# Kernel optimization log

Hardware: AMD Instinct MI355X
Metric: run time of the kernel (lower is better)

The kernel has to match this reference:

```python
import jax, jax.numpy as jnp
import numpy as np

PATCH = 3
ALPHA = 0.1


def _unfold3x3(x):
    # x: [B, C, H, W] -> [B, C*9, H, W], torch F.unfold with k=3, pad=1, stride=1
    B, C, H, W = x.shape
    p = PATCH // 2
    xp = jnp.pad(x, ((0, 0), (0, 0), (p, p), (p, p)))
    shifts = [xp[:, :, i:i + H, j:j + W] for i in range(PATCH) for j in range(PATCH)]
    # torch unfold orders (C, kh, kw); ordering is irrelevant for the dot-product
    # correlation, but we match it anyway: stack kernel positions after channel.
    out = jnp.stack(shifts, axis=2)  # [B, C, 9, H, W]
    return out.reshape(B, C * PATCH * PATCH, H, W)


def setup_inputs() -> dict:
    key = jax.random.key(0)
    k1, k2 = jax.random.split(key)
    x_lab = jax.random.normal(k1, (4, 3, 64, 64), dtype=jnp.float32)
    feature = jax.random.normal(k2, (4, 64, 64, 64), dtype=jnp.float32)
    return {"x_lab": x_lab, "feature": feature}


def reference(x_lab, feature):
    # scale_factor=1 and feature already at (H, W): both interpolates are identity.
    B, _, H, W = x_lab.shape
    N = H * W
    x_ab = x_lab.reshape(B, 3, N).transpose(0, 2, 1)          # [B, N, 3]
    lf = _unfold3x3(feature).reshape(B, -1, N)                 # [B, C*9, N]
    corr = jnp.einsum('bcn,bcm->bnm', lf, lf)                  # [B, N, N]
    attn = jax.nn.softmax(corr / ALPHA, axis=-1)
    weighted = jnp.einsum('bnm,bmc->bnc', attn, x_ab)          # [B, N, 3]
    return weighted.transpose(0, 2, 1).reshape(B, 3, H, W)
```

## Files before the change

kernel.cpp:

```cpp
#include <hip/hip_runtime.h>


#define NPIX 4096
#define ROWCH 528
#define ROWB  (ROWCH * 16)
#define SCALE 10.0f

typedef __attribute__((ext_vector_type(8))) short bf16x8;
typedef __attribute__((ext_vector_type(4))) float f32x4;

#define MF(a, b, c) __builtin_amdgcn_mfma_f32_16x16x32_bf16(a, b, c, 0, 0, 0)

__device__ __forceinline__ uint4 pack8(const float* v) {
    unsigned h[8];
#pragma unroll
    for (int j = 0; j < 8; ++j) {
        unsigned u = __float_as_uint(v[j]);
        u = u + 0x7fffu + ((u >> 16) & 1u);
        h[j] = u >> 16;
    }
    return (uint4){h[0] | (h[1] << 16), h[2] | (h[3] << 16),
                   h[4] | (h[5] << 16), h[6] | (h[7] << 16)};
}

__device__ __forceinline__ void load_row(const float* fr, int kc, int x, float* L) {
#pragma unroll
    for (int j = 0; j < 8; ++j) L[j] = fr[(size_t)(kc * 8 + j) * NPIX + x];
}

#define MFMA_GRP(T, DBASE) do {                                               \
    _Pragma("unroll")                                                         \
    for (int dx = 0; dx < 3; ++dx)                                            \
        _Pragma("unroll")                                                     \
        for (int ks = 0; ks < 2; ++ks) {                                      \
            acc[T][0] = MF(AF[((DBASE) + dx) * 2 + ks], Bf[ks][0][dx], acc[T][0]); \
            acc[T][1] = MF(AF[((DBASE) + dx) * 2 + ks], Bf[ks][1][dx], acc[T][1]); \
        }                                                                     \
} while (0)

#define RETIRE(S, myv) do {                                                   \
    _Pragma("unroll")                                                         \
    for (int kt = 0; kt < 2; ++kt) {                                          \
        const int kx = kh * 32 + kt * 16 + nl;                                \
        const float xv0 = xls[(myv) * 64 + kx];                               \
        const float xv1 = xls[NPIX + (myv) * 64 + kx];                        \
        const float xv2 = xls[2 * NPIX + (myv) * 64 + kx];                    \
        _Pragma("unroll")                                                     \
        for (int rg = 0; rg < 4; ++rg) {                                      \
            const float e = __expf(fmaf(acc[S][kt][rg], SCALE, negM[rg]));    \
            l_[rg] += e;                                                      \
            A0[rg] = fmaf(e, xv0, A0[rg]);                                    \
            A1[rg] = fmaf(e, xv1, A1[rg]);                                    \
            A2[rg] = fmaf(e, xv2, A2[rg]);                                    \
        }                                                                     \
        acc[S][kt] = (f32x4){0.f, 0.f, 0.f, 0.f};                             \
    }                                                                         \
} while (0)

#define STEP(RM, SN, SR, rr) do {                                             \
    const int r_ = (rr);                                                      \
    if (r_ <= 61) *(uint4*)(ring + (SR) * ROWB + wu16) = pack8(L);            \
    if (r_ <= 60) load_row(featb + (r_ + 3) * 64, kc, x, L);                  \
    if (r_ < 64) {                                                            \
        const char* base = ring + (RM) * ROWB + bu;                           \
        bf16x8 Bf[2][2][3];                                                   \
        _Pragma("unroll")                                                     \
        for (int ks = 0; ks < 2; ++ks)                                        \
            _Pragma("unroll")                                                 \
            for (int kt = 0; kt < 2; ++kt) {                                  \
                const char* p = base + (ks * 264 + kt * 16) * 16;             \
                Bf[ks][kt][0] = *(const bf16x8*)(p);                          \
                Bf[ks][kt][1] = *(const bf16x8*)(p + 16);                     \
                Bf[ks][kt][2] = *(const bf16x8*)(p + 32);                     \
            }                                                                 \
        if (r_ >= 1)     MFMA_GRP(SR, 6);           \
        MFMA_GRP(RM, 3);                                    \
        if (r_ + 1 < 64) MFMA_GRP(SN, 0);                   \
    }                                                                         \
    if (r_ >= 1 && r_ <= 64) RETIRE(SR, r_ - 1);                              \
    if (r_ < 64) __syncthreads();                                             \
} while (0)

__global__ __launch_bounds__(512)
__attribute__((amdgpu_waves_per_eu(2, 2)))
void nlwa_fused(const float* __restrict__ x_lab,
                const float* __restrict__ feature,
                float* __restrict__ out)
{
    __shared__ __align__(16) char ring[3 * ROWB];
    __shared__ float xls[3 * NPIX];
    __shared__ float part[3][8][64];
    __shared__ float ssq[3][64];
    __shared__ float4 scrF[64][2];

    const int tid = threadIdx.x;
    const int b = blockIdx.x >> 6, ny = blockIdx.x & 63;
    const int w = tid >> 6, lane = tid & 63;
    const int quad = lane >> 4, nl = lane & 15;
    const int qw = w & 3, kh = w >> 2;
    const int kc = w, x = lane;
    const int wu16 = (kc * 66 + x + 1) * 16;
    const int bu = (quad * 66 + kh * 32 + nl) * 16;

    const float* featb = feature + (size_t)b * 64 * NPIX;
    const float* xb = x_lab + (size_t)b * 3 * NPIX;

    {
        const float4* s4 = (const float4*)xb;
        float4* d4 = (float4*)xls;
        for (int i = tid; i < 3 * NPIX / 4; i += 512) d4[i] = s4[i];
    }
    if (tid < 48) {
        const int sl = tid / 16, pu = tid % 16;
        const int u = (pu >> 1) * 66 + (pu & 1) * 65;
        *(uint4*)(ring + sl * ROWB + u * 16) = (uint4){0u, 0u, 0u, 0u};
    }

    float L[8];
#pragma unroll
    for (int dyi = 0; dyi < 3; ++dyi) {
        const int qr = ny + dyi - 1;
        float ss = 0.f;
        if (qr >= 0 && qr < 64) {
            load_row(featb + qr * 64, kc, x, L);
#pragma unroll
            for (int j = 0; j < 8; ++j) ss = fmaf(L[j], L[j], ss);
            *(uint4*)(ring + dyi * ROWB + wu16) = pack8(L);
        } else {
            *(uint4*)(ring + dyi * ROWB + wu16) = (uint4){0u, 0u, 0u, 0u};
        }
        part[dyi][kc][x] = ss;
    }
    __syncthreads();

    if (tid < 192) {
        const int dyi = tid >> 6, xx = tid & 63;
        float s = 0.f;
#pragma unroll
        for (int k = 0; k < 8; ++k) s += part[dyi][k][xx];
        ssq[dyi][xx] = s;
    }

    bf16x8 AF[18];
#pragma unroll
    for (int dyi = 0; dyi < 3; ++dyi)
#pragma unroll
        for (int dx = 0; dx < 3; ++dx)
#pragma unroll
            for (int ks = 0; ks < 2; ++ks)
                AF[(dyi * 3 + dx) * 2 + ks] = *(const bf16x8*)(ring + dyi * ROWB +
                    ((quad + ks * 4) * 66 + qw * 16 + nl + dx) * 16);
    __syncthreads();

    float negM[4];
#pragma unroll
    for (int rg = 0; rg < 4; ++rg) {
        const int q = qw * 16 + quad * 4 + rg;
        float a = 0.f;
#pragma unroll
        for (int dyi = 0; dyi < 3; ++dyi)
#pragma unroll
            for (int dx = -1; dx <= 1; ++dx) {
                const int cx = q + dx;
                a += (cx >= 0 && cx < 64) ? ssq[dyi][cx] : 0.f;
            }
        negM[rg] = -SCALE * a;
    }

#pragma unroll
    for (int rr = 0; rr < 2; ++rr) {
        load_row(featb + rr * 64, kc, x, L);
        *(uint4*)(ring + rr * ROWB + wu16) = pack8(L);
    }
    load_row(featb + 2 * 64, kc, x, L);

    float l_[4], A0[4], A1[4], A2[4];
#pragma unroll
    for (int rg = 0; rg < 4; ++rg) { l_[rg] = 0.f; A0[rg] = 0.f; A1[rg] = 0.f; A2[rg] = 0.f; }
    f32x4 acc[3][2];
#pragma unroll
    for (int i = 0; i < 3; ++i) {
        acc[i][0] = (f32x4){0.f, 0.f, 0.f, 0.f};
        acc[i][1] = (f32x4){0.f, 0.f, 0.f, 0.f};
    }
    __syncthreads();

    for (int rb = 0; rb < 66; rb += 3) {
        STEP(0, 1, 2, rb);
        STEP(1, 2, 0, rb + 1);
        STEP(2, 0, 1, rb + 2);
    }

#pragma unroll
    for (int rg = 0; rg < 4; ++rg) {
#pragma unroll
        for (int off = 8; off >= 1; off >>= 1) {
            l_[rg] += __shfl_down(l_[rg], off, 16);
            A0[rg] += __shfl_down(A0[rg], off, 16);
            A1[rg] += __shfl_down(A1[rg], off, 16);
            A2[rg] += __shfl_down(A2[rg], off, 16);
        }
    }
    if (nl == 0) {
#pragma unroll
        for (int rg = 0; rg < 4; ++rg) {
            const int q = qw * 16 + quad * 4 + rg;
            scrF[q][kh] = make_float4(l_[rg], A0[rg], A1[rg], A2[rg]);
        }
    }
    __syncthreads();
    if (tid < 64) {
        const float4 t0 = scrF[tid][0], t1 = scrF[tid][1];
        const float inv = 1.0f / (t0.x + t1.x);
        float* o = out + (size_t)b * 3 * NPIX + ny * 64 + tid;
        o[0]        = (t0.y + t1.y) * inv;
        o[NPIX]     = (t0.z + t1.z) * inv;
        o[2 * NPIX] = (t0.w + t1.w) * inv;
    }
}

extern "C" void kernel_launch(void* const* d_in, const int* in_sizes, int n_in,
                              void* d_out, int out_size, void* d_ws, size_t ws_size,
                              hipStream_t stream) {
    (void)in_sizes; (void)n_in; (void)out_size; (void)d_ws; (void)ws_size;
    const float* x_lab   = (const float*)d_in[0];
    const float* feature = (const float*)d_in[1];
    float* out = (float*)d_out;
    nlwa_fused<<<dim3(256), dim3(512), 0, stream>>>(x_lab, feature, out);
}
```

Before: 134.3 us.

## Split key rows across two blocks per query row and combine partials

Each query row is now handled by two blocks, each covering half of the key rows (32 of 64). Each block writes unnormalized softmax sums and weighted accumulators to the workspace, and a second small kernel adds the two halves and normalizes. This doubles the grid from 256 to 512 blocks to fill more of the CUs, and the waves-per-EU hint is raised to match. The cost is a second launch, a workspace round trip, and recomputing the halo and norms in both halves. Because the max is a fixed bound taken from the norms, the two partial sums can be added directly.

```diff
diff --git a/kernel.cpp b/kernel.cpp
--- a/kernel.cpp
+++ b/kernel.cpp
@@ -5,6 +5,7 @@
 #define ROWCH 528
 #define ROWB  (ROWCH * 16)
 #define SCALE 10.0f
+#define XCH   2048
 
 typedef __attribute__((ext_vector_type(8))) short bf16x8;
 typedef __attribute__((ext_vector_type(4))) float f32x4;
@@ -43,8 +44,8 @@
     for (int kt = 0; kt < 2; ++kt) {                                          \
         const int kx = kh * 32 + kt * 16 + nl;                                \
         const float xv0 = xls[(myv) * 64 + kx];                               \
-        const float xv1 = xls[NPIX + (myv) * 64 + kx];                        \
-        const float xv2 = xls[2 * NPIX + (myv) * 64 + kx];                    \
+        const float xv1 = xls[XCH + (myv) * 64 + kx];                         \
+        const float xv2 = xls[2 * XCH + (myv) * 64 + kx];                     \
         _Pragma("unroll")                                                     \
         for (int rg = 0; rg < 4; ++rg) {                                      \
             const float e = __expf(fmaf(acc[S][kt][rg], SCALE, negM[rg]));    \
@@ -57,11 +58,15 @@
     }                                                                         \
 } while (0)
 
-#define STEP(RM, SN, SR, rr) do {                                             \
-    const int r_ = (rr);                                                      \
-    if (r_ <= 61) *(uint4*)(ring + (SR) * ROWB + wu16) = pack8(L);            \
-    if (r_ <= 60) load_row(featb + (r_ + 3) * 64, kc, x, L);                  \
-    if (r_ < 64) {                                                            \
+#define STEP(RM, SN, SR, tt) do {                                             \
+    const int t_ = (tt);                                                      \
+    if (t_ <= 31) *(uint4*)(ring + (SR) * ROWB + wu16) = pack8(L);            \
+    if (t_ <= 30) {                                                           \
+        const int g3 = K0 + 2 + t_;                                           \
+        if (g3 < 64) { load_row(featb + g3 * 64, kc, x, L); }                 \
+        else { _Pragma("unroll") for (int j = 0; j < 8; ++j) L[j] = 0.f; }    \
+    }                                                                         \
+    if (t_ <= 33) {                                                           \
         const char* base = ring + (RM) * ROWB + bu;                           \
         bf16x8 Bf[2][2][3];                                                   \
         _Pragma("unroll")                                                     \
@@ -73,28 +78,31 @@
                 Bf[ks][kt][1] = *(const bf16x8*)(p + 16);                     \
                 Bf[ks][kt][2] = *(const bf16x8*)(p + 32);                     \
             }                                                                 \
-        if (r_ >= 1)     MFMA_GRP(SR, 6);           \
-        MFMA_GRP(RM, 3);                                    \
-        if (r_ + 1 < 64) MFMA_GRP(SN, 0);                   \
+        if (t_ >= 2)              MFMA_GRP(SR, 6);    \
+        if (t_ >= 1 && t_ <= 32)  MFMA_GRP(RM, 3);          \
+        if (t_ <= 31)             MFMA_GRP(SN, 0);          \
     }                                                                         \
-    if (r_ >= 1 && r_ <= 64) RETIRE(SR, r_ - 1);                              \
-    if (r_ < 64) __syncthreads();                                             \
+    if (t_ >= 2 && t_ <= 33) RETIRE(SR, t_ - 2);                              \
+    if (t_ <= 33) __syncthreads();                                            \
 } while (0)
 
 __global__ __launch_bounds__(512)
-__attribute__((amdgpu_waves_per_eu(2, 2)))
+__attribute__((amdgpu_waves_per_eu(4, 4)))
 void nlwa_fused(const float* __restrict__ x_lab,
                 const float* __restrict__ feature,
-                float* __restrict__ out)
+                float4* __restrict__ ws)
 {
     __shared__ __align__(16) char ring[3 * ROWB];
-    __shared__ float xls[3 * NPIX];
+    __shared__ float xls[3 * XCH];
     __shared__ float part[3][8][64];
     __shared__ float ssq[3][64];
     __shared__ float4 scrF[64][2];
 
     const int tid = threadIdx.x;
-    const int b = blockIdx.x >> 6, ny = blockIdx.x & 63;
+    const int b = blockIdx.x >> 7;
+    const int r7 = blockIdx.x & 127;
+    const int ny = r7 >> 1, half = r7 & 1;
+    const int K0 = half * 32;
     const int w = tid >> 6, lane = tid & 63;
     const int quad = lane >> 4, nl = lane & 15;
     const int qw = w & 3, kh = w >> 2;
@@ -106,9 +114,12 @@
     const float* xb = x_lab + (size_t)b * 3 * NPIX;
 
     {
-        const float4* s4 = (const float4*)xb;
+        const int base = K0 * 64;
         float4* d4 = (float4*)xls;
-        for (int i = tid; i < 3 * NPIX / 4; i += 512) d4[i] = s4[i];
+        for (int i = tid; i < 3 * XCH / 4; i += 512) {
+            const int ch = i >> 9, off = i & 511;
+            d4[i] = *(const float4*)(xb + (size_t)ch * NPIX + base + off * 4);
+        }
     }
     if (tid < 48) {
         const int sl = tid / 16, pu = tid % 16;
@@ -169,10 +180,15 @@
 
 #pragma unroll
     for (int rr = 0; rr < 2; ++rr) {
-        load_row(featb + rr * 64, kc, x, L);
-        *(uint4*)(ring + rr * ROWB + wu16) = pack8(L);
-    }
-    load_row(featb + 2 * 64, kc, x, L);
+        const int g = K0 - 1 + rr;
+        if (g >= 0) {
+            load_row(featb + g * 64, kc, x, L);
+            *(uint4*)(ring + rr * ROWB + wu16) = pack8(L);
+        } else {
+            *(uint4*)(ring + rr * ROWB + wu16) = (uint4){0u, 0u, 0u, 0u};
+        }
+    }
+    load_row(featb + (K0 + 1) * 64, kc, x, L);
 
     float l_[4], A0[4], A1[4], A2[4];
 #pragma unroll
@@ -185,7 +201,7 @@
     }
     __syncthreads();
 
-    for (int rb = 0; rb < 66; rb += 3) {
+    for (int rb = 0; rb < 36; rb += 3) {
         STEP(0, 1, 2, rb);
         STEP(1, 2, 0, rb + 1);
         STEP(2, 0, 1, rb + 2);
@@ -211,20 +227,33 @@
     __syncthreads();
     if (tid < 64) {
         const float4 t0 = scrF[tid][0], t1 = scrF[tid][1];
-        const float inv = 1.0f / (t0.x + t1.x);
-        float* o = out + (size_t)b * 3 * NPIX + ny * 64 + tid;
-        o[0]        = (t0.y + t1.y) * inv;
-        o[NPIX]     = (t0.z + t1.z) * inv;
-        o[2 * NPIX] = (t0.w + t1.w) * inv;
-    }
+        ws[(size_t)blockIdx.x * 64 + tid] =
+            make_float4(t0.x + t1.x, t0.y + t1.y, t0.z + t1.z, t0.w + t1.w);
+    }
+}
+
+__global__ __launch_bounds__(256)
+void nlwa_combine(const float4* __restrict__ ws, float* __restrict__ out)
+{
+    const int i = blockIdx.x * 256 + threadIdx.x;
+    const int b = i >> 12, ny = (i >> 6) & 63, q = i & 63;
+    const float4 p0 = ws[(size_t)(((b * 64 + ny) * 2) + 0) * 64 + q];
+    const float4 p1 = ws[(size_t)(((b * 64 + ny) * 2) + 1) * 64 + q];
+    const float inv = 1.0f / (p0.x + p1.x);
+    float* o = out + (size_t)b * 3 * NPIX + ny * 64 + q;
+    o[0]        = (p0.y + p1.y) * inv;
+    o[NPIX]     = (p0.z + p1.z) * inv;
+    o[2 * NPIX] = (p0.w + p1.w) * inv;
 }
 
 extern "C" void kernel_launch(void* const* d_in, const int* in_sizes, int n_in,
                               void* d_out, int out_size, void* d_ws, size_t ws_size,
                               hipStream_t stream) {
-    (void)in_sizes; (void)n_in; (void)out_size; (void)d_ws; (void)ws_size;
+    (void)in_sizes; (void)n_in; (void)out_size; (void)ws_size;
     const float* x_lab   = (const float*)d_in[0];
     const float* feature = (const float*)d_in[1];
     float* out = (float*)d_out;
-    nlwa_fused<<<dim3(256), dim3(512), 0, stream>>>(x_lab, feature, out);
-}
+    float4* ws = (float4*)d_ws;
+    nlwa_fused<<<dim3(512), dim3(512), 0, stream>>>(x_lab, feature, ws);
+    nlwa_combine<<<dim3(64), dim3(256), 0, stream>>>(ws, out);
+}
```

New measurement: 372.4 us. 177% more time.
